# Optimization experiments

Measured on AMD Instinct MI355X. Metric: run time of the kernel, lower is better.

## Reference

```python
import jax, jax.numpy as jnp
import numpy as np

B, S, D, F, E, TOP_K = 2, 2048, 1024, 2048, 8, 2


def setup_inputs() -> dict:
    key = jax.random.key(0)
    k0, k1, k2, k3 = jax.random.split(key, 4)
    return {
        "hidden_states": jax.random.normal(k0, (B, S, D), jnp.float32),
        "gate_w": jax.random.normal(k1, (E, D), jnp.float32) * 0.02,   # torch Linear weight [out=E, in=D]
        "w1": jax.random.normal(k2, (E, D, F), jnp.float32) * 0.02,    # per-expert up-proj
        "w2": jax.random.normal(k3, (E, F, D), jnp.float32) * 0.02,    # per-expert down-proj
    }


def reference(hidden_states, gate_w, w1, w2):
    b, s, d = hidden_states.shape
    e = gate_w.shape[0]
    x = hidden_states.reshape(-1, d)                 # [T, D]
    t = x.shape[0]
    router_logits = x @ gate_w.T                     # [T, E]
    # softmax in fp32 as in original, then renormalized top-k weights
    probs = jax.nn.softmax(router_logits.astype(jnp.float32), axis=-1)
    topw, sel = jax.lax.top_k(probs, TOP_K)          # [T, K]
    topw = topw / jnp.sum(topw, axis=-1, keepdims=True)
    topw = topw.astype(x.dtype)
    # dense combine weights: zero for unselected experts (top_k indices are distinct)
    combine = jnp.zeros((t, e), x.dtype).at[jnp.arange(t)[:, None], sel].add(topw)  # [T, E]
    out = jnp.zeros_like(x)
    for ei in range(e):  # small fixed expert count
        h = jax.nn.silu(x @ w1[ei]) @ w2[ei]         # [T, D]
        out = out + combine[:, ei:ei + 1] * h
    return out.reshape(b, s, d), router_logits
```

## Files before the change

### kernel.cpp

```cpp
#include <hip/hip_runtime.h>
#include <hip/hip_bf16.h>
#include <math.h>

#define Tt 4096
#define Dd 1024
#define Ff 2048
#define Ee 8

typedef unsigned short u16;
typedef short bf16x8 __attribute__((ext_vector_type(8)));
typedef float f32x4 __attribute__((ext_vector_type(4)));

__device__ __forceinline__ u16 f2bf(float f) {
  union { float f; unsigned u; } v; v.f = f;
  unsigned r = v.u + 0x7fffu + ((v.u >> 16) & 1u);
  return (u16)(r >> 16);
}

__device__ __forceinline__ void gload16(const void* g, void* l) {
  __builtin_amdgcn_global_load_lds(
      (const __attribute__((address_space(1))) unsigned int*)g,
      (__attribute__((address_space(3))) unsigned int*)l, 16, 0, 0);
}

__global__ __launch_bounds__(256) void router_kernel(
    const float* __restrict__ x, const float* __restrict__ gw,
    float* __restrict__ logits)
{
  int t = blockIdx.x * 4 + (threadIdx.x >> 6);
  int lane = threadIdx.x & 63;
  const float* xr = x + (size_t)t * Dd;
  float xv[16];
#pragma unroll
  for (int i = 0; i < 4; ++i) {
    float4 v = *reinterpret_cast<const float4*>(xr + lane * 16 + i * 4);
    xv[i*4+0] = v.x; xv[i*4+1] = v.y; xv[i*4+2] = v.z; xv[i*4+3] = v.w;
  }
#pragma unroll
  for (int e = 0; e < Ee; ++e) {
    const float* gr = gw + (size_t)e * Dd + lane * 16;
    float s = 0.f;
#pragma unroll
    for (int i = 0; i < 4; ++i) {
      float4 g = *reinterpret_cast<const float4*>(gr + i * 4);
      s += xv[i*4+0]*g.x + xv[i*4+1]*g.y + xv[i*4+2]*g.z + xv[i*4+3]*g.w;
    }
#pragma unroll
    for (int o = 32; o > 0; o >>= 1) s += __shfl_xor(s, o);
    if (lane == 0) logits[(size_t)t * Ee + e] = s;
  }
}

__global__ __launch_bounds__(256) void build_kernel(
    const float* __restrict__ logits, int* __restrict__ meta,
    int* __restrict__ list, float* __restrict__ wgt)
{
  __shared__ int hist[8], cur[8];
  const int tid = threadIdx.x;
  const int lane = tid & 63;
  if (tid < 8) hist[tid] = 0;
  __syncthreads();
  for (int it = 0; it < Tt / 256; ++it) {
    int t = it * 256 + tid;
    float4 lo = *reinterpret_cast<const float4*>(logits + (size_t)t * 8);
    float4 hi = *reinterpret_cast<const float4*>(logits + (size_t)t * 8 + 4);
    float s[8] = {lo.x, lo.y, lo.z, lo.w, hi.x, hi.y, hi.z, hi.w};
    int i1 = 0; float m1 = s[0];
#pragma unroll
    for (int e = 1; e < 8; ++e) if (s[e] > m1) { m1 = s[e]; i1 = e; }
    int i2 = -1; float m2 = -__builtin_inff();
#pragma unroll
    for (int e = 0; e < 8; ++e) if (e != i1 && s[e] > m2) { m2 = s[e]; i2 = e; }
#pragma unroll
    for (int k = 0; k < 2; ++k) {
      int gg = k ? i2 : i1;
      unsigned long long m = ~0ull;
#pragma unroll
      for (int b = 0; b < 3; ++b) {
        unsigned long long vb = __ballot((gg >> b) & 1);
        m &= ((gg >> b) & 1) ? vb : ~vb;
      }
      int rank = __popcll(m & ((1ull << lane) - 1));
      if (rank == 0) atomicAdd(&hist[gg], __popcll(m));
    }
  }
  __syncthreads();
  if (tid == 0) {
    int sacc = 0;
    for (int g = 0; g < 8; ++g) {
      meta[g] = hist[g];
      meta[32 + g] = sacc;
      cur[g] = sacc;
      sacc += hist[g];
    }
  }
  __syncthreads();
  for (int it = 0; it < Tt / 256; ++it) {
    int t = it * 256 + tid;
    float4 lo = *reinterpret_cast<const float4*>(logits + (size_t)t * 8);
    float4 hi = *reinterpret_cast<const float4*>(logits + (size_t)t * 8 + 4);
    float s[8] = {lo.x, lo.y, lo.z, lo.w, hi.x, hi.y, hi.z, hi.w};
    int i1 = 0; float m1 = s[0];
#pragma unroll
    for (int e = 1; e < 8; ++e) if (s[e] > m1) { m1 = s[e]; i1 = e; }
    int i2 = -1; float m2 = -__builtin_inff();
#pragma unroll
    for (int e = 0; e < 8; ++e) if (e != i1 && s[e] > m2) { m2 = s[e]; i2 = e; }
    float wa = 1.f / (1.f + expf(m2 - m1));
#pragma unroll
    for (int k = 0; k < 2; ++k) {
      int gg = k ? i2 : i1;
      float w = k ? (1.f - wa) : wa;
      unsigned long long m = ~0ull;
#pragma unroll
      for (int b = 0; b < 3; ++b) {
        unsigned long long vb = __ballot((gg >> b) & 1);
        m &= ((gg >> b) & 1) ? vb : ~vb;
      }
      int rank = __popcll(m & ((1ull << lane) - 1));
      int ldr = __ffsll(m) - 1;
      int base = 0;
      if (rank == 0) base = atomicAdd(&cur[gg], __popcll(m));
      base = __shfl(base, ldr);
      list[base + rank] = t;
      wgt[base + rank] = w;
    }
  }
}

__global__ __launch_bounds__(256) void cvt_bf16_kernel(
    const float* __restrict__ in, u16* __restrict__ out, int n4)
{
  int i = blockIdx.x * 256 + threadIdx.x;
  if (i >= n4) return;
  float4 v = reinterpret_cast<const float4*>(in)[i];
  ushort4 b;
  b.x = f2bf(v.x); b.y = f2bf(v.y); b.z = f2bf(v.z); b.w = f2bf(v.w);
  reinterpret_cast<ushort4*>(out)[i] = b;
}

__global__ __launch_bounds__(256) void transpose_bf16_kernel(
    const float* __restrict__ in, u16* __restrict__ out, int R, int C)
{
  __shared__ u16 st[64][65];
  const size_t eoff = (size_t)blockIdx.z * R * C;
  const float* ip = in + eoff;
  u16* op = out + eoff;
  int r0 = blockIdx.y * 64, c0 = blockIdx.x * 64;
  int t = threadIdx.x;
  int rr = t >> 2;
  int cb = (t & 3) * 16;
#pragma unroll
  for (int i = 0; i < 4; ++i) {
    float4 v = *reinterpret_cast<const float4*>(ip + (size_t)(r0 + rr) * C + c0 + cb + i * 4);
    st[rr][cb + i*4 + 0] = f2bf(v.x);
    st[rr][cb + i*4 + 1] = f2bf(v.y);
    st[rr][cb + i*4 + 2] = f2bf(v.z);
    st[rr][cb + i*4 + 3] = f2bf(v.w);
  }
  __syncthreads();
#pragma unroll
  for (int i = 0; i < 4; ++i) {
    ushort4 b;
    b.x = st[cb + i*4 + 0][rr];
    b.y = st[cb + i*4 + 1][rr];
    b.z = st[cb + i*4 + 2][rr];
    b.w = st[cb + i*4 + 3][rr];
    *reinterpret_cast<ushort4*>(op + (size_t)(c0 + rr) * R + r0 + cb + i * 4) = b;
  }
}

template<int MODE, int N_, int K_>
__global__ __launch_bounds__(256) void gemm_g(
    const u16* __restrict__ Abase, const u16* __restrict__ Bbase,
    void* __restrict__ Cout, const int* __restrict__ meta,
    const int* __restrict__ list, const float* __restrict__ wgt)
{
  constexpr int BM = 128, BN = 128;
  constexpr int NXc = N_ / BN;
  constexpr int NYc = 32;
  constexpr int NWG = NXc * NYc * 8;
  constexpr int CPX = NWG / 8;
  constexpr int ABUF = BM * 32, BBUF = BN * 32;

  __shared__ u16 Al[2 * ABUF];
  __shared__ u16 Bl[2 * BBUF];

  const int orig = blockIdx.x + NXc * (blockIdx.y + NYc * blockIdx.z);
  const int swz  = (orig & 7) * CPX + (orig >> 3);
  const int bz   = swz / (NXc * NYc);
  const int rem  = swz - bz * (NXc * NYc);
  const int by   = rem / NXc;
  const int bx   = rem - by * NXc;

  const int e   = bz;
  const int cnt = meta[e];
  if (by * BM >= cnt) return;
  const int off = meta[32 + e];

  const int tid  = threadIdx.x;
  const int lane = tid & 63;
  const int wave = tid >> 6;
  const int wr   = wave >> 1, wc = wave & 1;
  const int n0   = bx * BN;

  const int l4 = lane >> 2;
  const int kc = (lane & 3) * 8;

  const u16* aptr[2];
  u16* alds[2];
#pragma unroll
  for (int c = 0; c < 2; ++c) {
    int chunk = wave * 2 + c;
    int row = chunk * 16 + l4;
    int i = by * BM + row;
    if (i >= cnt) i = cnt - 1;
    int srow = (MODE == 0) ? list[off + i] : (off + i);
    aptr[c] = Abase + (size_t)srow * K_ + kc;
    alds[c] = Al + chunk * 512;
  }
  const u16* bptr[2];
  u16* blds[2];
#pragma unroll
  for (int c = 0; c < 2; ++c) {
    int chunk = wave * 2 + c;
    int row = chunk * 16 + l4;
    bptr[c] = Bbase + ((size_t)e * N_ + n0 + row) * K_ + kc;
    blds[c] = Bl + chunk * 512;
  }

  f32x4 acc[4][4] = {};
  const int r16 = lane & 15;
  const int kq  = (lane >> 4) * 8;
  constexpr int NT = K_ / 32;

#pragma unroll
  for (int c = 0; c < 2; ++c) gload16(aptr[c], alds[c]);
#pragma unroll
  for (int c = 0; c < 2; ++c) gload16(bptr[c], blds[c]);
  __syncthreads();

  int cur = 0;
  for (int t = 0; t < NT; ++t) {
    if (t + 1 < NT) {
      int k0 = (t + 1) * 32;
      int nb = cur ^ 1;
#pragma unroll
      for (int c = 0; c < 2; ++c) gload16(aptr[c] + k0, alds[c] + nb * ABUF);
#pragma unroll
      for (int c = 0; c < 2; ++c) gload16(bptr[c] + k0, blds[c] + nb * BBUF);
    }
    const u16* Ab = Al + cur * ABUF;
    const u16* Bb = Bl + cur * BBUF;
    bf16x8 af[4], bfv[4];
#pragma unroll
    for (int m = 0; m < 4; ++m)
      af[m] = *reinterpret_cast<const bf16x8*>(&Ab[(wr*64 + m*16 + r16) * 32 + kq]);
#pragma unroll
    for (int n = 0; n < 4; ++n)
      bfv[n] = *reinterpret_cast<const bf16x8*>(&Bb[(wc*64 + n*16 + r16) * 32 + kq]);
#pragma unroll
    for (int m = 0; m < 4; ++m)
#pragma unroll
      for (int n = 0; n < 4; ++n)
        acc[m][n] = __builtin_amdgcn_mfma_f32_16x16x32_bf16(af[m], bfv[n], acc[m][n], 0, 0, 0);
    __syncthreads();
    cur ^= 1;
  }

  const int colb = n0 + wc * 64 + r16;
  const int rb4  = wr * 64 + ((lane >> 4) << 2);
#pragma unroll
  for (int m = 0; m < 4; ++m) {
#pragma unroll
    for (int r = 0; r < 4; ++r) {
      int i = by * BM + rb4 + m * 16 + r;
      if (i >= cnt) continue;
      if (MODE == 0) {
        u16* hp = (u16*)Cout + (size_t)(off + i) * N_;
#pragma unroll
        for (int n = 0; n < 4; ++n) {
          float v = acc[m][n][r];
          v = v / (1.f + expf(-v));
          hp[colb + n * 16] = f2bf(v);
        }
      } else {
        int   tok = list[off + i];
        float w   = wgt[off + i];
        float* o = (float*)Cout + (size_t)tok * N_;
#pragma unroll
        for (int n = 0; n < 4; ++n)
          atomicAdd(&o[colb + n * 16], w * acc[m][n][r]);
      }
    }
  }
}

__global__ __launch_bounds__(256) void combine_kernel(
    const float* __restrict__ logits, float* __restrict__ combine)
{
  int t = blockIdx.x * 256 + threadIdx.x;
  if (t >= Tt) return;
  float4 lo = *reinterpret_cast<const float4*>(logits + (size_t)t * 8);
  float4 hi = *reinterpret_cast<const float4*>(logits + (size_t)t * 8 + 4);
  float s[8] = {lo.x, lo.y, lo.z, lo.w, hi.x, hi.y, hi.z, hi.w};
  int i1 = 0; float m1 = s[0];
#pragma unroll
  for (int e = 1; e < 8; ++e) if (s[e] > m1) { m1 = s[e]; i1 = e; }
  int i2 = -1; float m2 = -__builtin_inff();
#pragma unroll
  for (int e = 0; e < 8; ++e) if (e != i1 && s[e] > m2) { m2 = s[e]; i2 = e; }
  float wa = 1.f / (1.f + expf(m2 - m1));
#pragma unroll
  for (int e = 0; e < 8; ++e)
    combine[(size_t)t * 8 + e] = (e == i1) ? wa : ((e == i2) ? (1.f - wa) : 0.f);
}

template<int MODE, int N_, int K_>
__global__ __launch_bounds__(256) void gemm_dense(
    const float* __restrict__ A, const float* __restrict__ Bg,
    float* __restrict__ C, const float* __restrict__ combine,
    int expert, int first)
{
  constexpr int BM = 128, BN = 128, BK = 32, LDT = 40;
  __shared__ u16 Al[BM * LDT];
  __shared__ u16 Bl[BN * LDT];
  const int tid  = threadIdx.x;
  const int lane = tid & 63;
  const int wave = tid >> 6;
  const int wr = wave >> 1, wc = wave & 1;
  const int m0 = blockIdx.y * BM;
  const int n0 = blockIdx.x * BN;
  f32x4 acc[4][4] = {};
  for (int k0 = 0; k0 < K_; k0 += BK) {
#pragma unroll
    for (int i = 0; i < 4; ++i) {
      int f = tid + 256 * i;
      int row = f >> 3;
      int c4 = (f & 7) << 2;
      float4 v = *reinterpret_cast<const float4*>(A + (size_t)(m0 + row) * K_ + k0 + c4);
      ushort4 b;
      b.x = f2bf(v.x); b.y = f2bf(v.y); b.z = f2bf(v.z); b.w = f2bf(v.w);
      *reinterpret_cast<ushort4*>(&Al[row * LDT + c4]) = b;
    }
    {
      int n  = tid & 127;
      int kb = (tid >> 7) << 4;
      const float* bp = Bg + (size_t)(k0 + kb) * N_ + n0 + n;
      u16 tmp[16];
#pragma unroll
      for (int kk = 0; kk < 16; ++kk)
        tmp[kk] = f2bf(bp[(size_t)kk * N_]);
      u16* p = &Bl[n * LDT + kb];
#pragma unroll
      for (int i = 0; i < 4; ++i) {
        ushort4 b;
        b.x = tmp[i*4+0]; b.y = tmp[i*4+1]; b.z = tmp[i*4+2]; b.w = tmp[i*4+3];
        *reinterpret_cast<ushort4*>(p + i * 4) = b;
      }
    }
    __syncthreads();
    bf16x8 af[4], bfr[4];
    const int kq  = (lane >> 4) << 3;
    const int r16 = lane & 15;
#pragma unroll
    for (int m = 0; m < 4; ++m)
      af[m] = *reinterpret_cast<const bf16x8*>(&Al[(wr*64 + m*16 + r16) * LDT + kq]);
#pragma unroll
    for (int n = 0; n < 4; ++n)
      bfr[n] = *reinterpret_cast<const bf16x8*>(&Bl[(wc*64 + n*16 + r16) * LDT + kq]);
#pragma unroll
    for (int m = 0; m < 4; ++m)
#pragma unroll
      for (int n = 0; n < 4; ++n)
        acc[m][n] = __builtin_amdgcn_mfma_f32_16x16x32_bf16(af[m], bfr[n], acc[m][n], 0, 0, 0);
    __syncthreads();
  }
  const int col0 = n0 + wc * 64 + (lane & 15);
  const int rbs  = m0 + wr * 64 + ((lane >> 4) << 2);
#pragma unroll
  for (int m = 0; m < 4; ++m) {
#pragma unroll
    for (int r = 0; r < 4; ++r) {
      int row = rbs + m * 16 + r;
      if (MODE == 0) {
#pragma unroll
        for (int n = 0; n < 4; ++n) {
          float v = acc[m][n][r];
          v = v / (1.f + expf(-v));
          C[(size_t)row * N_ + col0 + n * 16] = v;
        }
      } else {
        float w = combine[(size_t)row * Ee + expert];
        if (first) {
#pragma unroll
          for (int n = 0; n < 4; ++n)
            C[(size_t)row * N_ + col0 + n * 16] = w * acc[m][n][r];
        } else {
#pragma unroll
          for (int n = 0; n < 4; ++n)
            C[(size_t)row * N_ + col0 + n * 16] += w * acc[m][n][r];
        }
      }
    }
  }
}

extern "C" void kernel_launch(void* const* d_in, const int* in_sizes, int n_in,
                              void* d_out, int out_size, void* d_ws, size_t ws_size,
                              hipStream_t stream)
{
  const float* x  = (const float*)d_in[0];
  const float* gw = (const float*)d_in[1];
  const float* w1 = (const float*)d_in[2];
  const float* w2 = (const float*)d_in[3];
  float* out    = (float*)d_out;
  float* logits = out + (size_t)Tt * Dd;

  int*   meta = (int*)d_ws;
  int*   list = (int*)((char*)d_ws + 256);
  float* wgt  = (float*)((char*)d_ws + 256 + 32768);
  u16*   xb   = (u16*)((char*)d_ws + 262144);
  u16*   h1   = (u16*)((char*)d_ws + 262144 + 8388608);
  u16*   wT   = (u16*)((char*)d_ws + 262144 + 8388608 + 33554432);
  const size_t NEED = 262144ull + 8388608ull + 33554432ull + 33554432ull;

  router_kernel<<<Tt / 4, 256, 0, stream>>>(x, gw, logits);

  if (ws_size >= NEED) {
    hipMemsetAsync(out, 0, (size_t)Tt * Dd * sizeof(float), stream);
    build_kernel<<<1, 256, 0, stream>>>(logits, meta, list, wgt);
    cvt_bf16_kernel<<<(Tt * Dd / 4) / 256, 256, 0, stream>>>(x, xb, Tt * Dd / 4);
    transpose_bf16_kernel<<<dim3(Ff/64, Dd/64, Ee), 256, 0, stream>>>(w1, wT, Dd, Ff);
    gemm_g<0, Ff, Dd><<<dim3(Ff/128, 32, 8), 256, 0, stream>>>(xb, wT, h1, meta, list, wgt);
    transpose_bf16_kernel<<<dim3(Dd/64, Ff/64, Ee), 256, 0, stream>>>(w2, wT, Ff, Dd);
    gemm_g<1, Dd, Ff><<<dim3(Dd/128, 32, 8), 256, 0, stream>>>(h1, wT, out, meta, list, wgt);
  } else {
    float* combine = (float*)d_ws;
    float* h1d     = combine + (size_t)Tt * Ee;
    combine_kernel<<<Tt / 256, 256, 0, stream>>>(logits, combine);
    size_t cb = (size_t)Tt * Ee * sizeof(float);
    size_t avail = ws_size > cb ? (ws_size - cb) : 0;
    long maxrows = (long)(avail / ((size_t)Ff * sizeof(float)));
    int chunk = (maxrows >= Tt) ? Tt : (int)((maxrows / 128) * 128);
    if (chunk < 128) chunk = 128;
    for (int c0 = 0; c0 < Tt; c0 += chunk) {
      int rows = (Tt - c0) < chunk ? (Tt - c0) : chunk;
      for (int e = 0; e < Ee; ++e) {
        gemm_dense<0, Ff, Dd><<<dim3(Ff/128, rows/128), 256, 0, stream>>>(
            x + (size_t)c0 * Dd, w1 + (size_t)e * Dd * Ff, h1d, nullptr, e, 0);
        gemm_dense<1, Dd, Ff><<<dim3(Dd/128, rows/128), 256, 0, stream>>>(
            h1d, w2 + (size_t)e * Ff * Dd, out + (size_t)c0 * Dd,
            combine + (size_t)c0 * Ee, e, (e == 0) ? 1 : 0);
      }
    }
  }
}
```

Baseline: 217.8 us.

## Add split-K to down-proj GEMM and deepen LDS prefetch pipeline

The grouped GEMM gains a KSPLIT template parameter. The down-projection launches with K split in two across twice as many workgroups, raising parallelism and improving load balance. The main loop now preloads two stages and uses explicit vmcnt/lgkmcnt waits with raw barriers. The load for tile t+2 is issued after fragment reads so global-to-LDS traffic overlaps the MFMAs. This adds twice as many atomic accumulations into the output, and the hand-tuned waitcnts risk being fragile.

```diff
diff --git a/kernel.cpp b/kernel.cpp
--- a/kernel.cpp
+++ b/kernel.cpp
@@ -170,7 +170,7 @@
   }
 }
 
-template<int MODE, int N_, int K_>
+template<int MODE, int N_, int K_, int KSPLIT>
 __global__ __launch_bounds__(256) void gemm_g(
     const u16* __restrict__ Abase, const u16* __restrict__ Bbase,
     void* __restrict__ Cout, const int* __restrict__ meta,
@@ -179,9 +179,11 @@
   constexpr int BM = 128, BN = 128;
   constexpr int NXc = N_ / BN;
   constexpr int NYc = 32;
-  constexpr int NWG = NXc * NYc * 8;
-  constexpr int CPX = NWG / 8;
+  constexpr int NZc = 8 * KSPLIT;
+  constexpr int CPX = NXc * NYc * KSPLIT;
   constexpr int ABUF = BM * 32, BBUF = BN * 32;
+  constexpr int KLOC = K_ / KSPLIT;
+  constexpr int NT = KLOC / 32;
 
   __shared__ u16 Al[2 * ABUF];
   __shared__ u16 Bl[2 * BBUF];
@@ -193,7 +195,8 @@
   const int by   = rem / NXc;
   const int bx   = rem - by * NXc;
 
-  const int e   = bz;
+  const int e   = bz / KSPLIT;
+  const int kh  = bz - e * KSPLIT;
   const int cnt = meta[e];
   if (by * BM >= cnt) return;
   const int off = meta[32 + e];
@@ -203,6 +206,7 @@
   const int wave = tid >> 6;
   const int wr   = wave >> 1, wc = wave & 1;
   const int n0   = bx * BN;
+  const int kbase = kh * KLOC;
 
   const int l4 = lane >> 2;
   const int kc = (lane & 3) * 8;
@@ -216,7 +220,7 @@
     int i = by * BM + row;
     if (i >= cnt) i = cnt - 1;
     int srow = (MODE == 0) ? list[off + i] : (off + i);
-    aptr[c] = Abase + (size_t)srow * K_ + kc;
+    aptr[c] = Abase + (size_t)srow * K_ + kbase + kc;
     alds[c] = Al + chunk * 512;
   }
   const u16* bptr[2];
@@ -225,31 +229,30 @@
   for (int c = 0; c < 2; ++c) {
     int chunk = wave * 2 + c;
     int row = chunk * 16 + l4;
-    bptr[c] = Bbase + ((size_t)e * N_ + n0 + row) * K_ + kc;
+    bptr[c] = Bbase + ((size_t)e * N_ + n0 + row) * K_ + kbase + kc;
     blds[c] = Bl + chunk * 512;
   }
 
   f32x4 acc[4][4] = {};
   const int r16 = lane & 15;
   const int kq  = (lane >> 4) * 8;
-  constexpr int NT = K_ / 32;
 
 #pragma unroll
   for (int c = 0; c < 2; ++c) gload16(aptr[c], alds[c]);
 #pragma unroll
   for (int c = 0; c < 2; ++c) gload16(bptr[c], blds[c]);
-  __syncthreads();
+#pragma unroll
+  for (int c = 0; c < 2; ++c) gload16(aptr[c] + 32, alds[c] + ABUF);
+#pragma unroll
+  for (int c = 0; c < 2; ++c) gload16(bptr[c] + 32, blds[c] + BBUF);
 
   int cur = 0;
   for (int t = 0; t < NT; ++t) {
-    if (t + 1 < NT) {
-      int k0 = (t + 1) * 32;
-      int nb = cur ^ 1;
-#pragma unroll
-      for (int c = 0; c < 2; ++c) gload16(aptr[c] + k0, alds[c] + nb * ABUF);
-#pragma unroll
-      for (int c = 0; c < 2; ++c) gload16(bptr[c] + k0, blds[c] + nb * BBUF);
-    }
+    if (t < NT - 1) asm volatile("s_waitcnt vmcnt(4)" ::: "memory");
+    else            asm volatile("s_waitcnt vmcnt(0)" ::: "memory");
+    __builtin_amdgcn_s_barrier();
+    __builtin_amdgcn_sched_barrier(0);
+
     const u16* Ab = Al + cur * ABUF;
     const u16* Bb = Bl + cur * BBUF;
     bf16x8 af[4], bfv[4];
@@ -259,12 +262,22 @@
 #pragma unroll
     for (int n = 0; n < 4; ++n)
       bfv[n] = *reinterpret_cast<const bf16x8*>(&Bb[(wc*64 + n*16 + r16) * 32 + kq]);
+    asm volatile("s_waitcnt lgkmcnt(0)" ::: "memory");
+    __builtin_amdgcn_sched_barrier(0);
+    __builtin_amdgcn_s_barrier();
+
+    if (t + 2 < NT) {
+      int k0 = (t + 2) * 32;
+#pragma unroll
+      for (int c = 0; c < 2; ++c) gload16(aptr[c] + k0, alds[c] + cur * ABUF);
+#pragma unroll
+      for (int c = 0; c < 2; ++c) gload16(bptr[c] + k0, blds[c] + cur * BBUF);
+    }
 #pragma unroll
     for (int m = 0; m < 4; ++m)
 #pragma unroll
       for (int n = 0; n < 4; ++n)
         acc[m][n] = __builtin_amdgcn_mfma_f32_16x16x32_bf16(af[m], bfv[n], acc[m][n], 0, 0, 0);
-    __syncthreads();
     cur ^= 1;
   }
 
@@ -432,9 +445,9 @@
     build_kernel<<<1, 256, 0, stream>>>(logits, meta, list, wgt);
     cvt_bf16_kernel<<<(Tt * Dd / 4) / 256, 256, 0, stream>>>(x, xb, Tt * Dd / 4);
     transpose_bf16_kernel<<<dim3(Ff/64, Dd/64, Ee), 256, 0, stream>>>(w1, wT, Dd, Ff);
-    gemm_g<0, Ff, Dd><<<dim3(Ff/128, 32, 8), 256, 0, stream>>>(xb, wT, h1, meta, list, wgt);
+    gemm_g<0, Ff, Dd, 1><<<dim3(Ff/128, 32, 8), 256, 0, stream>>>(xb, wT, h1, meta, list, wgt);
     transpose_bf16_kernel<<<dim3(Dd/64, Ff/64, Ee), 256, 0, stream>>>(w2, wT, Ff, Dd);
-    gemm_g<1, Dd, Ff><<<dim3(Dd/128, 32, 8), 256, 0, stream>>>(h1, wT, out, meta, list, wgt);
+    gemm_g<1, Dd, Ff, 2><<<dim3(Dd/128, 32, 16), 256, 0, stream>>>(h1, wT, out, meta, list, wgt);
   } else {
     float* combine = (float*)d_ws;
     float* h1d     = combine + (size_t)Tt * Ee;
```

Result: slower. 226.7 us (+4.1%).

## Use two-wave 64x128 warp tiles in grouped GEMM and fuse bf16 cast into router

Applied to the files above, without the earlier changes.

The grouped expert GEMM now runs 128 threads per block. Each wave computes a 64x128 sub-tile (4x8 MFMA accumulators) instead of 64x64, and the LDS staging layout changes to row-within-chunk order to match the fragment reads. This cuts LDS fragment loads per MFMA, but doubles per-wave accumulator registers and halves the waves available per tile for hiding latency. Separately, the bf16 conversion of activations moves into the router kernel, dropping one kernel launch and one full read of x. In the fallback path, though, that conversion writes into the workspace without a size check.

```diff
diff --git a/kernel.cpp b/kernel.cpp
--- a/kernel.cpp
+++ b/kernel.cpp
@@ -25,7 +25,7 @@
 
 __global__ __launch_bounds__(256) void router_kernel(
     const float* __restrict__ x, const float* __restrict__ gw,
-    float* __restrict__ logits)
+    float* __restrict__ logits, u16* __restrict__ xb)
 {
   int t = blockIdx.x * 4 + (threadIdx.x >> 6);
   int lane = threadIdx.x & 63;
@@ -35,6 +35,13 @@
   for (int i = 0; i < 4; ++i) {
     float4 v = *reinterpret_cast<const float4*>(xr + lane * 16 + i * 4);
     xv[i*4+0] = v.x; xv[i*4+1] = v.y; xv[i*4+2] = v.z; xv[i*4+3] = v.w;
+  }
+#pragma unroll
+  for (int i = 0; i < 4; ++i) {
+    ushort4 b;
+    b.x = f2bf(xv[i*4+0]); b.y = f2bf(xv[i*4+1]);
+    b.z = f2bf(xv[i*4+2]); b.w = f2bf(xv[i*4+3]);
+    *reinterpret_cast<ushort4*>(xb + (size_t)t * Dd + lane * 16 + i * 4) = b;
   }
 #pragma unroll
   for (int e = 0; e < Ee; ++e) {
@@ -128,17 +135,6 @@
   }
 }
 
-__global__ __launch_bounds__(256) void cvt_bf16_kernel(
-    const float* __restrict__ in, u16* __restrict__ out, int n4)
-{
-  int i = blockIdx.x * 256 + threadIdx.x;
-  if (i >= n4) return;
-  float4 v = reinterpret_cast<const float4*>(in)[i];
-  ushort4 b;
-  b.x = f2bf(v.x); b.y = f2bf(v.y); b.z = f2bf(v.z); b.w = f2bf(v.w);
-  reinterpret_cast<ushort4*>(out)[i] = b;
-}
-
 __global__ __launch_bounds__(256) void transpose_bf16_kernel(
     const float* __restrict__ in, u16* __restrict__ out, int R, int C)
 {
@@ -171,20 +167,19 @@
 }
 
 template<int MODE, int N_, int K_>
-__global__ __launch_bounds__(256) void gemm_g(
+__global__ __launch_bounds__(128) void gemm_g(
     const u16* __restrict__ Abase, const u16* __restrict__ Bbase,
     void* __restrict__ Cout, const int* __restrict__ meta,
     const int* __restrict__ list, const float* __restrict__ wgt)
 {
-  constexpr int BM = 128, BN = 128;
-  constexpr int NXc = N_ / BN;
+  constexpr int NXc = N_ / 128;
   constexpr int NYc = 32;
-  constexpr int NWG = NXc * NYc * 8;
-  constexpr int CPX = NWG / 8;
-  constexpr int ABUF = BM * 32, BBUF = BN * 32;
-
-  __shared__ u16 Al[2 * ABUF];
-  __shared__ u16 Bl[2 * BBUF];
+  constexpr int CPX = NXc * NYc;
+  constexpr int BUF = 128 * 32;
+  constexpr int NT  = K_ / 32;
+
+  __shared__ u16 Al[2 * BUF];
+  __shared__ u16 Bl[2 * BUF];
 
   const int orig = blockIdx.x + NXc * (blockIdx.y + NYc * blockIdx.z);
   const int swz  = (orig & 7) * CPX + (orig >> 3);
@@ -195,49 +190,42 @@
 
   const int e   = bz;
   const int cnt = meta[e];
-  if (by * BM >= cnt) return;
+  if (by * 128 >= cnt) return;
   const int off = meta[32 + e];
 
   const int tid  = threadIdx.x;
   const int lane = tid & 63;
   const int wave = tid >> 6;
-  const int wr   = wave >> 1, wc = wave & 1;
-  const int n0   = bx * BN;
-
-  const int l4 = lane >> 2;
-  const int kc = (lane & 3) * 8;
-
-  const u16* aptr[2];
-  u16* alds[2];
-#pragma unroll
-  for (int c = 0; c < 2; ++c) {
-    int chunk = wave * 2 + c;
-    int row = chunk * 16 + l4;
-    int i = by * BM + row;
+  const int n0   = bx * 128;
+  const int lr   = lane & 15;
+  const int lp   = lane >> 4;
+
+  const u16* aptr[4];
+  u16* alds[4];
+#pragma unroll
+  for (int c = 0; c < 4; ++c) {
+    int chunk = wave * 4 + c;
+    int i = by * 128 + chunk * 16 + lr;
     if (i >= cnt) i = cnt - 1;
     int srow = (MODE == 0) ? list[off + i] : (off + i);
-    aptr[c] = Abase + (size_t)srow * K_ + kc;
+    aptr[c] = Abase + (size_t)srow * K_ + lp * 8;
     alds[c] = Al + chunk * 512;
   }
-  const u16* bptr[2];
-  u16* blds[2];
-#pragma unroll
-  for (int c = 0; c < 2; ++c) {
-    int chunk = wave * 2 + c;
-    int row = chunk * 16 + l4;
-    bptr[c] = Bbase + ((size_t)e * N_ + n0 + row) * K_ + kc;
+  const u16* bptr[4];
+  u16* blds[4];
+#pragma unroll
+  for (int c = 0; c < 4; ++c) {
+    int chunk = wave * 4 + c;
+    bptr[c] = Bbase + ((size_t)e * N_ + n0 + chunk * 16 + lr) * K_ + lp * 8;
     blds[c] = Bl + chunk * 512;
   }
 
-  f32x4 acc[4][4] = {};
-  const int r16 = lane & 15;
-  const int kq  = (lane >> 4) * 8;
-  constexpr int NT = K_ / 32;
-
-#pragma unroll
-  for (int c = 0; c < 2; ++c) gload16(aptr[c], alds[c]);
-#pragma unroll
-  for (int c = 0; c < 2; ++c) gload16(bptr[c], blds[c]);
+  f32x4 acc[4][8] = {};
+
+#pragma unroll
+  for (int c = 0; c < 4; ++c) gload16(aptr[c], alds[c]);
+#pragma unroll
+  for (int c = 0; c < 4; ++c) gload16(bptr[c], blds[c]);
   __syncthreads();
 
   int cur = 0;
@@ -246,51 +234,49 @@
       int k0 = (t + 1) * 32;
       int nb = cur ^ 1;
 #pragma unroll
-      for (int c = 0; c < 2; ++c) gload16(aptr[c] + k0, alds[c] + nb * ABUF);
-#pragma unroll
-      for (int c = 0; c < 2; ++c) gload16(bptr[c] + k0, blds[c] + nb * BBUF);
-    }
-    const u16* Ab = Al + cur * ABUF;
-    const u16* Bb = Bl + cur * BBUF;
-    bf16x8 af[4], bfv[4];
+      for (int c = 0; c < 4; ++c) gload16(aptr[c] + k0, alds[c] + nb * BUF);
+#pragma unroll
+      for (int c = 0; c < 4; ++c) gload16(bptr[c] + k0, blds[c] + nb * BUF);
+    }
+    const u16* Ab = Al + cur * BUF;
+    const u16* Bb = Bl + cur * BUF;
+    bf16x8 af[4], bfv[8];
 #pragma unroll
     for (int m = 0; m < 4; ++m)
-      af[m] = *reinterpret_cast<const bf16x8*>(&Ab[(wr*64 + m*16 + r16) * 32 + kq]);
-#pragma unroll
-    for (int n = 0; n < 4; ++n)
-      bfv[n] = *reinterpret_cast<const bf16x8*>(&Bb[(wc*64 + n*16 + r16) * 32 + kq]);
+      af[m] = *reinterpret_cast<const bf16x8*>(&Ab[(wave*4 + m) * 512 + lp * 128 + lr * 8]);
+#pragma unroll
+    for (int n = 0; n < 8; ++n)
+      bfv[n] = *reinterpret_cast<const bf16x8*>(&Bb[n * 512 + lp * 128 + lr * 8]);
 #pragma unroll
     for (int m = 0; m < 4; ++m)
 #pragma unroll
-      for (int n = 0; n < 4; ++n)
+      for (int n = 0; n < 8; ++n)
         acc[m][n] = __builtin_amdgcn_mfma_f32_16x16x32_bf16(af[m], bfv[n], acc[m][n], 0, 0, 0);
     __syncthreads();
     cur ^= 1;
   }
 
-  const int colb = n0 + wc * 64 + r16;
-  const int rb4  = wr * 64 + ((lane >> 4) << 2);
 #pragma unroll
   for (int m = 0; m < 4; ++m) {
 #pragma unroll
     for (int r = 0; r < 4; ++r) {
-      int i = by * BM + rb4 + m * 16 + r;
-      if (i >= cnt) continue;
+      int islot = by * 128 + wave * 64 + m * 16 + lp * 4 + r;
+      if (islot >= cnt) continue;
       if (MODE == 0) {
-        u16* hp = (u16*)Cout + (size_t)(off + i) * N_;
-#pragma unroll
-        for (int n = 0; n < 4; ++n) {
+        u16* hp = (u16*)Cout + (size_t)(off + islot) * N_;
+#pragma unroll
+        for (int n = 0; n < 8; ++n) {
           float v = acc[m][n][r];
           v = v / (1.f + expf(-v));
-          hp[colb + n * 16] = f2bf(v);
+          hp[n0 + n * 16 + lr] = f2bf(v);
         }
       } else {
-        int   tok = list[off + i];
-        float w   = wgt[off + i];
+        int   tok = list[off + islot];
+        float w   = wgt[off + islot];
         float* o = (float*)Cout + (size_t)tok * N_;
 #pragma unroll
-        for (int n = 0; n < 4; ++n)
-          atomicAdd(&o[colb + n * 16], w * acc[m][n][r]);
+        for (int n = 0; n < 8; ++n)
+          atomicAdd(&o[n0 + n * 16 + lr], w * acc[m][n][r]);
       }
     }
   }
@@ -425,19 +411,19 @@
   u16*   wT   = (u16*)((char*)d_ws + 262144 + 8388608 + 33554432);
   const size_t NEED = 262144ull + 8388608ull + 33554432ull + 33554432ull;
 
-  router_kernel<<<Tt / 4, 256, 0, stream>>>(x, gw, logits);
-
   if (ws_size >= NEED) {
+    router_kernel<<<Tt / 4, 256, 0, stream>>>(x, gw, logits, xb);
     hipMemsetAsync(out, 0, (size_t)Tt * Dd * sizeof(float), stream);
     build_kernel<<<1, 256, 0, stream>>>(logits, meta, list, wgt);
-    cvt_bf16_kernel<<<(Tt * Dd / 4) / 256, 256, 0, stream>>>(x, xb, Tt * Dd / 4);
     transpose_bf16_kernel<<<dim3(Ff/64, Dd/64, Ee), 256, 0, stream>>>(w1, wT, Dd, Ff);
-    gemm_g<0, Ff, Dd><<<dim3(Ff/128, 32, 8), 256, 0, stream>>>(xb, wT, h1, meta, list, wgt);
+    gemm_g<0, Ff, Dd><<<dim3(Ff/128, 32, 8), 128, 0, stream>>>(xb, wT, h1, meta, list, wgt);
     transpose_bf16_kernel<<<dim3(Dd/64, Ff/64, Ee), 256, 0, stream>>>(w2, wT, Ff, Dd);
-    gemm_g<1, Dd, Ff><<<dim3(Dd/128, 32, 8), 256, 0, stream>>>(h1, wT, out, meta, list, wgt);
+    gemm_g<1, Dd, Ff><<<dim3(Dd/128, 32, 8), 128, 0, stream>>>(h1, wT, out, meta, list, wgt);
   } else {
     float* combine = (float*)d_ws;
     float* h1d     = combine + (size_t)Tt * Ee;
+    u16* dummy = (u16*)d_ws;
+    router_kernel<<<Tt / 4, 256, 0, stream>>>(x, gw, logits, (u16*)((char*)d_ws));
     combine_kernel<<<Tt / 256, 256, 0, stream>>>(logits, combine);
     size_t cb = (size_t)Tt * Ee * sizeof(float);
     size_t avail = ws_size > cb ? (ws_size - cb) : 0;
```

Result: slower. 323.6 us (+48.6%).
